# Kernel optimization log

Hardware: AMD Instinct MI355X
Metric: run time of the kernel (lower is better)

Reference implementation:

```python
import jax, jax.numpy as jnp
import numpy as np

E = 1024   # embedding_dim
A = 1024   # attention_dim
H = 16     # num_heads
D = A // H # head_dim


def setup_inputs() -> dict:
    key = jax.random.key(0)
    ks = jax.random.split(key, 9)
    s = 1.0 / np.sqrt(E)
    so = 1.0 / np.sqrt(A)
    return {
        "x": jax.random.normal(ks[0], (2, 2048, E), dtype=jnp.float32),
        "Wq": jax.random.uniform(ks[1], (E, A), jnp.float32, -s, s),
        "bq": jax.random.uniform(ks[2], (A,), jnp.float32, -s, s),
        "Wk": jax.random.uniform(ks[3], (E, A), jnp.float32, -s, s),
        "bk": jax.random.uniform(ks[4], (A,), jnp.float32, -s, s),
        "Wv": jax.random.uniform(ks[5], (E, A), jnp.float32, -s, s),
        "bv": jax.random.uniform(ks[6], (A,), jnp.float32, -s, s),
        "Wo": jax.random.uniform(ks[7], (A, E), jnp.float32, -so, so),
        "bo": jax.random.uniform(ks[8], (E,), jnp.float32, -so, so),
    }


def reference(x, Wq, bq, Wk, bk, Wv, bv, Wo, bo):
    B, S, _ = x.shape
    # projections -> [B, H, S, D]
    def split_heads(t):
        return t.reshape(B, S, H, D).transpose(0, 2, 1, 3)
    Q = split_heads(x @ Wq + bq)
    K = split_heads(x @ Wk + bk)
    V = split_heads(x @ Wv + bv)
    scores = jnp.einsum("bhqd,bhkd->bhqk", Q, K) / jnp.sqrt(jnp.float32(D))
    causal = jnp.tril(jnp.ones((S, S), dtype=bool))
    scores = jnp.where(causal, scores, -jnp.inf)
    attn = jax.nn.softmax(scores, axis=-1)  # dropout p=0 (eval/deterministic)
    ctx = jnp.einsum("bhqk,bhkd->bhqd", attn, V)
    ctx = ctx.transpose(0, 2, 1, 3).reshape(B, S, A)
    out = ctx @ Wo + bo
    return (out, attn)
```

## Files before the change

### kernel.cpp

```cpp
#include <hip/hip_runtime.h>
#include <cstddef>

typedef __bf16 bf16_t;
typedef __attribute__((ext_vector_type(8))) __bf16 bf16x8;
typedef __attribute__((ext_vector_type(4))) float f32x4;

#define BATCH 2
#define SEQ   2048
#define EMB   1024
#define ADIM  1024
#define NHEAD 16
#define HDIM  64
#define MROWS 4096

__device__ inline unsigned short f2bf(float f) {
    bf16_t b = (bf16_t)f;
    return __builtin_bit_cast(unsigned short, b);
}

__global__ __launch_bounds__(256) void convert_x_kernel(
    const float* __restrict__ in, unsigned short* __restrict__ out, int n8)
{
    int i = blockIdx.x * 256 + threadIdx.x;
    if (i >= n8) return;
    const float4* p = (const float4*)(in + (size_t)i * 8);
    float4 a = p[0], b = p[1];
    unsigned int w0 = f2bf(a.x) | ((unsigned)f2bf(a.y) << 16);
    unsigned int w1 = f2bf(a.z) | ((unsigned)f2bf(a.w) << 16);
    unsigned int w2 = f2bf(b.x) | ((unsigned)f2bf(b.y) << 16);
    unsigned int w3 = f2bf(b.z) | ((unsigned)f2bf(b.w) << 16);
    uint4 v = {w0, w1, w2, w3};
    *(uint4*)(out + (size_t)i * 8) = v;
}

__global__ __launch_bounds__(256) void transpose_w_kernel(
    const float* __restrict__ Wq, const float* __restrict__ Wk,
    const float* __restrict__ Wv, const float* __restrict__ Wo,
    unsigned short* __restrict__ Wt_qkv, unsigned short* __restrict__ Wt_o)
{
    __shared__ float tile[64][65];
    const int m = blockIdx.z;
    const float* W = (m == 0) ? Wq : (m == 1) ? Wk : (m == 2) ? Wv : Wo;
    unsigned short* dst = (m < 3) ? (Wt_qkv + (size_t)m * 1024 * 1024) : Wt_o;
    const int r0 = blockIdx.y * 64, c0 = blockIdx.x * 64;
    const int t = threadIdx.x;
    const int r = t >> 2, c4 = (t & 3) * 16;
    #pragma unroll
    for (int j = 0; j < 16; j += 4) {
        float4 v = *(const float4*)(W + (size_t)(r0 + r) * 1024 + c0 + c4 + j);
        tile[r][c4 + j + 0] = v.x;
        tile[r][c4 + j + 1] = v.y;
        tile[r][c4 + j + 2] = v.z;
        tile[r][c4 + j + 3] = v.w;
    }
    __syncthreads();
    const int oc = t >> 2, ch = (t & 3) * 16;
    unsigned int ww[8];
    #pragma unroll
    for (int j = 0; j < 16; j += 2)
        ww[j >> 1] = f2bf(tile[ch + j][oc]) | ((unsigned)f2bf(tile[ch + j + 1][oc]) << 16);
    unsigned short* o = dst + (size_t)(c0 + oc) * 1024 + r0 + ch;
    *(uint4*)(o) = *(uint4*)&ww[0];
    *(uint4*)(o + 8) = *(uint4*)&ww[4];
}

template<int EPI, int NBX, int NWG>
__global__ __launch_bounds__(256) void gemm_mfma_kernel(
    const unsigned short* __restrict__ A,
    const unsigned short* __restrict__ Bt,
    const float* __restrict__ b0, const float* __restrict__ b1, const float* __restrict__ b2,
    void* __restrict__ outp, unsigned short* __restrict__ vt)
{
    __shared__ __align__(16) unsigned short Asm[4096];
    __shared__ __align__(16) unsigned short Bsm[4096];
    const int tid = threadIdx.x, lane = tid & 63, w = tid >> 6;
    const int wr = w >> 1, wc = w & 1;

    const int lin = blockIdx.x;
    const int wg = (lin & 7) * (NWG >> 3) + (lin >> 3);
    const int stripe = wg / (8 * NBX);
    const int rem = wg % (8 * NBX);
    const int bx = rem >> 3;
    const int by = stripe * 8 + (rem & 7);

    const int rowBase = by * 128, colBase = bx * 128;
    const int K = 1024;

    f32x4 acc[4][4];
    #pragma unroll
    for (int i = 0; i < 4; ++i)
        #pragma unroll
        for (int j = 0; j < 4; ++j)
            acc[i][j] = (f32x4){0.f, 0.f, 0.f, 0.f};

    int mt_s[2], cc_s[2], r16_s[2];
    #pragma unroll
    for (int i = 0; i < 2; ++i) {
        int chunk = w * 128 + i * 64 + lane;
        mt_s[i] = chunk >> 6;
        cc_s[i] = (chunk & 63) >> 4;
        r16_s[i] = chunk & 15;
    }

    for (int k0 = 0; k0 < K; k0 += 32) {
        __syncthreads();
        #pragma unroll
        for (int i = 0; i < 2; ++i) {
            const unsigned short* ga = A + (size_t)(rowBase + mt_s[i] * 16 + r16_s[i]) * K + k0 + cc_s[i] * 8;
            __builtin_amdgcn_global_load_lds(
                (const __attribute__((address_space(1))) unsigned int*)ga,
                (__attribute__((address_space(3))) unsigned int*)(Asm + (size_t)(w * 128 + i * 64) * 8),
                16, 0, 0);
            const unsigned short* gb = Bt + (size_t)(colBase + mt_s[i] * 16 + r16_s[i]) * K + k0 + cc_s[i] * 8;
            __builtin_amdgcn_global_load_lds(
                (const __attribute__((address_space(1))) unsigned int*)gb,
                (__attribute__((address_space(3))) unsigned int*)(Bsm + (size_t)(w * 128 + i * 64) * 8),
                16, 0, 0);
        }
        __syncthreads();

        bf16x8 af[4], bfr[4];
        #pragma unroll
        for (int mt = 0; mt < 4; ++mt)
            af[mt] = *(const bf16x8*)(Asm + (size_t)((wr * 4 + mt) * 64 + lane) * 8);
        #pragma unroll
        for (int nt = 0; nt < 4; ++nt)
            bfr[nt] = *(const bf16x8*)(Bsm + (size_t)((wc * 4 + nt) * 64 + lane) * 8);
        #pragma unroll
        for (int mt = 0; mt < 4; ++mt)
            #pragma unroll
            for (int nt = 0; nt < 4; ++nt)
                acc[mt][nt] = __builtin_amdgcn_mfma_f32_16x16x32_bf16(af[mt], bfr[nt], acc[mt][nt], 0, 0, 0);
    }

    const int g = lane >> 4, r16 = lane & 15;
    const int seg = colBase >> 10;
    const float* bias = (seg == 0) ? b0 : (seg == 1) ? b1 : b2;

    if (EPI == 0) {
        unsigned short* qkv = (unsigned short*)outp;
        #pragma unroll
        for (int mt = 0; mt < 4; ++mt) {
            const int row0 = rowBase + wr * 64 + mt * 16 + 4 * g;
            #pragma unroll
            for (int nt = 0; nt < 4; ++nt) {
                const int col = colBase + wc * 64 + nt * 16 + r16;
                const float bb = bias[col & 1023];
                if (seg < 2) {
                    #pragma unroll
                    for (int rr = 0; rr < 4; ++rr)
                        qkv[(size_t)(row0 + rr) * 3072 + col] = f2bf(acc[mt][nt][rr] + bb);
                } else {
                    unsigned int p0 = f2bf(acc[mt][nt][0] + bb) | ((unsigned)f2bf(acc[mt][nt][1] + bb) << 16);
                    unsigned int p1 = f2bf(acc[mt][nt][2] + bb) | ((unsigned)f2bf(acc[mt][nt][3] + bb) << 16);
                    uint2 pv = {p0, p1};
                    *(uint2*)(vt + (size_t)(col - 2048) * 4096 + row0) = pv;
                }
            }
        }
    } else {
        float* out = (float*)outp;
        #pragma unroll
        for (int mt = 0; mt < 4; ++mt) {
            const int row0 = rowBase + wr * 64 + mt * 16 + 4 * g;
            #pragma unroll
            for (int nt = 0; nt < 4; ++nt) {
                const int col = colBase + wc * 64 + nt * 16 + r16;
                const float bb = bias[col];
                #pragma unroll
                for (int rr = 0; rr < 4; ++rr)
                    out[(size_t)(row0 + rr) * 1024 + col] = acc[mt][nt][rr] + bb;
            }
        }
    }
}

__global__ __launch_bounds__(256, 4) void attn_mfma_kernel(
    const unsigned short* __restrict__ qkv,
    const unsigned short* __restrict__ vt,
    float* __restrict__ attn,
    unsigned short* __restrict__ ctx)
{
    __shared__ __align__(16) unsigned short Ksm[2][4096];
    __shared__ __align__(16) unsigned short Vsm[2][4096];
    __shared__ __align__(16) unsigned short Psm[4][1024];

    const int j = blockIdx.x;
    const int xcd = j & 7, slot = j >> 3;
    const int bh = xcd + 8 * (slot & 3);
    const int s4 = slot >> 2;
    const int qt = 8 * (s4 >> 3) + (((s4 & 7) + 2 * (s4 >> 3)) & 7);
    const int b = bh >> 4, h = bh & 15;
    const int tid = threadIdx.x, lane = tid & 63, w = tid >> 6;
    const int g = lane >> 4, r16 = lane & 15;
    const int qrow0 = qt * 64 + w * 16;

    bf16x8 qf[2];
    #pragma unroll
    for (int k2 = 0; k2 < 2; ++k2)
        qf[k2] = *(const bf16x8*)(qkv + (size_t)(b * SEQ + qrow0 + r16) * 3072 + h * 64 + k2 * 32 + g * 8);

    const int sr = tid >> 2;
    const int sbc = (tid & 3) * 32;
    const int swz = (sr & 7) << 4;
    char* Kb = (char*)Ksm;
    char* Vb = (char*)Vsm;

    float rsum[4] = {0.f, 0.f, 0.f, 0.f};

    {
        const char* gk = (const char*)(qkv + (size_t)(b * SEQ + sr) * 3072 + 1024 + h * 64);
        uint4 a0 = *(const uint4*)(gk + sbc);
        uint4 a1 = *(const uint4*)(gk + sbc + 16);
        *(uint4*)(Kb + ((sr * 128 + sbc) ^ swz)) = a0;
        *(uint4*)(Kb + ((sr * 128 + sbc + 16) ^ swz)) = a1;
    }
    __syncthreads();
    for (int kt = 0; kt <= qt; ++kt) {
        const int cur = kt & 1;
        uint4 a0, a1;
        if (kt < qt) {
            const char* gk = (const char*)(qkv + (size_t)(b * SEQ + (kt + 1) * 64 + sr) * 3072 + 1024 + h * 64);
            a0 = *(const uint4*)(gk + sbc);
            a1 = *(const uint4*)(gk + sbc + 16);
        }
        const char* Kc = Kb + cur * 8192;
        #pragma unroll
        for (int nt = 0; nt < 4; ++nt) {
            f32x4 s = {0.f, 0.f, 0.f, 0.f};
            const int krow = nt * 16 + r16;
            #pragma unroll
            for (int k2 = 0; k2 < 2; ++k2) {
                bf16x8 kf = *(const bf16x8*)(Kc + ((krow * 128 + k2 * 64 + g * 16) ^ ((krow & 7) << 4)));
                s = __builtin_amdgcn_mfma_f32_16x16x32_bf16(qf[k2], kf, s, 0, 0, 0);
            }
            #pragma unroll
            for (int rr = 0; rr < 4; ++rr) {
                const int q = qrow0 + 4 * g + rr;
                const int k = kt * 64 + nt * 16 + r16;
                if (k <= q) rsum[rr] += __expf(s[rr] * 0.125f);
            }
        }
        if (kt < qt) {
            char* Kn = Kb + (cur ^ 1) * 8192;
            *(uint4*)(Kn + ((sr * 128 + sbc) ^ swz)) = a0;
            *(uint4*)(Kn + ((sr * 128 + sbc + 16) ^ swz)) = a1;
        }
        __syncthreads();
    }
    #pragma unroll
    for (int rr = 0; rr < 4; ++rr) {
        float v = rsum[rr];
        v += __shfl_xor(v, 1, 64);
        v += __shfl_xor(v, 2, 64);
        v += __shfl_xor(v, 4, 64);
        v += __shfl_xor(v, 8, 64);
        rsum[rr] = 1.0f / v;
    }

    f32x4 cacc[4];
    #pragma unroll
    for (int nt = 0; nt < 4; ++nt) cacc[nt] = (f32x4){0.f, 0.f, 0.f, 0.f};

    {
        const char* gk = (const char*)(qkv + (size_t)(b * SEQ + sr) * 3072 + 1024 + h * 64);
        uint4 a0 = *(const uint4*)(gk + sbc);
        uint4 a1 = *(const uint4*)(gk + sbc + 16);
        const char* gv = (const char*)(vt + (size_t)(h * 64 + sr) * 4096 + b * SEQ);
        uint4 v0 = *(const uint4*)(gv + sbc);
        uint4 v1 = *(const uint4*)(gv + sbc + 16);
        *(uint4*)(Kb + ((sr * 128 + sbc) ^ swz)) = a0;
        *(uint4*)(Kb + ((sr * 128 + sbc + 16) ^ swz)) = a1;
        *(uint4*)(Vb + ((sr * 128 + sbc) ^ swz)) = v0;
        *(uint4*)(Vb + ((sr * 128 + sbc + 16) ^ swz)) = v1;
    }
    __syncthreads();
    for (int kt = 0; kt <= qt; ++kt) {
        const int cur = kt & 1;
        const int kbase = kt * 64;
        uint4 a0, a1, v0, v1;
        if (kt < qt) {
            const char* gk = (const char*)(qkv + (size_t)(b * SEQ + kbase + 64 + sr) * 3072 + 1024 + h * 64);
            a0 = *(const uint4*)(gk + sbc);
            a1 = *(const uint4*)(gk + sbc + 16);
            const char* gv = (const char*)(vt + (size_t)(h * 64 + sr) * 4096 + b * SEQ + kbase + 64);
            v0 = *(const uint4*)(gv + sbc);
            v1 = *(const uint4*)(gv + sbc + 16);
        }
        const char* Kc = Kb + cur * 8192;
        const char* Vc = Vb + cur * 8192;

        #pragma unroll
        for (int nt = 0; nt < 4; ++nt) {
            f32x4 s = {0.f, 0.f, 0.f, 0.f};
            const int krow = nt * 16 + r16;
            #pragma unroll
            for (int k2 = 0; k2 < 2; ++k2) {
                bf16x8 kf = *(const bf16x8*)(Kc + ((krow * 128 + k2 * 64 + g * 16) ^ ((krow & 7) << 4)));
                s = __builtin_amdgcn_mfma_f32_16x16x32_bf16(qf[k2], kf, s, 0, 0, 0);
            }
            #pragma unroll
            for (int rr = 0; rr < 4; ++rr) {
                const int q = qrow0 + 4 * g + rr;
                const int k = kbase + nt * 16 + r16;
                float pn = 0.0f;
                if (k <= q) pn = __expf(s[rr] * 0.125f) * rsum[rr];
                attn[((size_t)bh * SEQ + q) * SEQ + k] = pn;
                const int prow = 4 * g + rr;
                *(unsigned short*)((char*)(Psm[w]) + ((prow * 128 + (nt * 16 + r16) * 2) ^ ((prow & 7) << 4))) = f2bf(pn);
            }
        }
        bf16x8 pf[2];
        #pragma unroll
        for (int k2 = 0; k2 < 2; ++k2)
            pf[k2] = *(const bf16x8*)((char*)(Psm[w]) + ((r16 * 128 + k2 * 64 + g * 16) ^ ((r16 & 7) << 4)));
        #pragma unroll
        for (int nt = 0; nt < 4; ++nt) {
            const int vrow = nt * 16 + r16;
            #pragma unroll
            for (int k2 = 0; k2 < 2; ++k2) {
                bf16x8 vf = *(const bf16x8*)(Vc + ((vrow * 128 + k2 * 64 + g * 16) ^ ((vrow & 7) << 4)));
                cacc[nt] = __builtin_amdgcn_mfma_f32_16x16x32_bf16(pf[k2], vf, cacc[nt], 0, 0, 0);
            }
        }
        if (kt < qt) {
            char* Kn = Kb + (cur ^ 1) * 8192;
            char* Vn = Vb + (cur ^ 1) * 8192;
            *(uint4*)(Kn + ((sr * 128 + sbc) ^ swz)) = a0;
            *(uint4*)(Kn + ((sr * 128 + sbc + 16) ^ swz)) = a1;
            *(uint4*)(Vn + ((sr * 128 + sbc) ^ swz)) = v0;
            *(uint4*)(Vn + ((sr * 128 + sbc + 16) ^ swz)) = v1;
        }
        __syncthreads();
    }

    #pragma unroll
    for (int nt = 0; nt < 4; ++nt)
        #pragma unroll
        for (int rr = 0; rr < 4; ++rr) {
            const int q = qrow0 + 4 * g + rr;
            ctx[(size_t)(b * SEQ + q) * 1024 + h * 64 + nt * 16 + r16] = f2bf(cacc[nt][rr]);
        }

    const int colStart = 64 * (qt + 1);
    const int Wc = SEQ - colStart;
    if (Wc > 0) {
        const int w4 = Wc >> 2;
        for (int c = tid; c < 64 * w4; c += 256) {
            const int row = qt * 64 + c / w4;
            const int col = colStart + (c % w4) * 4;
            *(float4*)(attn + ((size_t)bh * SEQ + row) * SEQ + col) = make_float4(0.f, 0.f, 0.f, 0.f);
        }
    }
}

extern "C" void kernel_launch(void* const* d_in, const int* in_sizes, int n_in,
                              void* d_out, int out_size, void* d_ws, size_t ws_size,
                              hipStream_t stream)
{
    const float* x  = (const float*)d_in[0];
    const float* Wq = (const float*)d_in[1];
    const float* bq = (const float*)d_in[2];
    const float* Wk = (const float*)d_in[3];
    const float* bk = (const float*)d_in[4];
    const float* Wv = (const float*)d_in[5];
    const float* bv = (const float*)d_in[6];
    const float* Wo = (const float*)d_in[7];
    const float* bo = (const float*)d_in[8];

    float* out  = (float*)d_out;
    float* attn = out + (size_t)BATCH * SEQ * EMB;

    unsigned short* xb     = (unsigned short*)d_ws;
    unsigned short* wt_qkv = xb + (size_t)MROWS * 1024;
    unsigned short* wt_o   = wt_qkv + (size_t)3072 * 1024;
    unsigned short* qkvb   = wt_o + (size_t)1024 * 1024;
    unsigned short* vtb    = qkvb + (size_t)MROWS * 3072;
    unsigned short* ctxb   = vtb + (size_t)1024 * MROWS;

    convert_x_kernel<<<2048, 256, 0, stream>>>(x, xb, MROWS * 1024 / 8);
    transpose_w_kernel<<<dim3(16, 16, 4), 256, 0, stream>>>(Wq, Wk, Wv, Wo, wt_qkv, wt_o);

    gemm_mfma_kernel<0, 24, 768><<<768, 256, 0, stream>>>(xb, wt_qkv, bq, bk, bv, qkvb, vtb);

    attn_mfma_kernel<<<1024, 256, 0, stream>>>(qkvb, vtb, attn, ctxb);

    gemm_mfma_kernel<1, 8, 256><<<256, 256, 0, stream>>>(ctxb, wt_o, bo, bo, bo, out, nullptr);
}
```

Baseline: 251.7 us.

## Split softmax row-sum pass into separate key-split kernel

Moves the first pass of the two-pass softmax (QK^T then exp row sums) out of the attention kernel into a new rowsum kernel. That kernel splits the key range into four chunks per query tile across a 3D grid and writes partial sums to workspace. The attention kernel then reads and combines the partials. This parallelises the causal first pass, which was serial and load-imbalanced in each block. In exchange it adds a kernel launch and reads K directly from global memory without LDS staging, and it skips the max-subtraction just as before.

```diff
diff --git a/kernel.cpp b/kernel.cpp
--- a/kernel.cpp
+++ b/kernel.cpp
@@ -175,9 +175,74 @@
     }
 }
 
+__global__ __launch_bounds__(256) void rowsum_kernel(
+    const unsigned short* __restrict__ qkv,
+    float* __restrict__ partial)
+{
+    const int bh = blockIdx.x, qt = blockIdx.y, ks = blockIdx.z;
+    const int b = bh >> 4, h = bh & 15;
+    const int tid = threadIdx.x, lane = tid & 63, w = tid >> 6;
+    const int g = lane >> 4, r16 = lane & 15;
+    float* pbase = partial + (((size_t)(bh * 32 + qt)) * 4 + ks) * 64;
+
+    if (ks * 8 > qt) {
+        if (tid < 64) pbase[tid] = 0.0f;
+        return;
+    }
+
+    const int qrow0 = qt * 64 + w * 16;
+    bf16x8 qf[2];
+    #pragma unroll
+    for (int k2 = 0; k2 < 2; ++k2)
+        qf[k2] = *(const bf16x8*)(qkv + (size_t)(b * SEQ + qrow0 + r16) * 3072 + h * 64 + k2 * 32 + g * 8);
+
+    float rsum[4] = {0.f, 0.f, 0.f, 0.f};
+    const int ktEnd = (ks * 8 + 8 < qt + 1) ? ks * 8 + 8 : qt + 1;
+    for (int kt = ks * 8; kt < ktEnd; ++kt) {
+        const unsigned short* kp = qkv + (size_t)(b * SEQ + kt * 64) * 3072 + 1024 + h * 64;
+        #pragma unroll
+        for (int nt = 0; nt < 4; ++nt) {
+            f32x4 s = {0.f, 0.f, 0.f, 0.f};
+            const int krow = nt * 16 + r16;
+            #pragma unroll
+            for (int k2 = 0; k2 < 2; ++k2) {
+                bf16x8 kf = *(const bf16x8*)(kp + (size_t)krow * 3072 + k2 * 32 + g * 8);
+                s = __builtin_amdgcn_mfma_f32_16x16x32_bf16(qf[k2], kf, s, 0, 0, 0);
+            }
+            if (kt < qt) {
+                #pragma unroll
+                for (int rr = 0; rr < 4; ++rr)
+                    rsum[rr] += __expf(s[rr] * 0.125f);
+            } else {
+                #pragma unroll
+                for (int rr = 0; rr < 4; ++rr) {
+                    const int q = qrow0 + 4 * g + rr;
+                    const int k = kt * 64 + nt * 16 + r16;
+                    if (k <= q) rsum[rr] += __expf(s[rr] * 0.125f);
+                }
+            }
+        }
+    }
+    #pragma unroll
+    for (int rr = 0; rr < 4; ++rr) {
+        float v = rsum[rr];
+        v += __shfl_xor(v, 1, 64);
+        v += __shfl_xor(v, 2, 64);
+        v += __shfl_xor(v, 4, 64);
+        v += __shfl_xor(v, 8, 64);
+        rsum[rr] = v;
+    }
+    if (r16 == 0) {
+        #pragma unroll
+        for (int rr = 0; rr < 4; ++rr)
+            pbase[w * 16 + 4 * g + rr] = rsum[rr];
+    }
+}
+
 __global__ __launch_bounds__(256, 4) void attn_mfma_kernel(
     const unsigned short* __restrict__ qkv,
     const unsigned short* __restrict__ vt,
+    const float* __restrict__ partial,
     float* __restrict__ attn,
     unsigned short* __restrict__ ctx)
 {
@@ -200,63 +265,19 @@
     for (int k2 = 0; k2 < 2; ++k2)
         qf[k2] = *(const bf16x8*)(qkv + (size_t)(b * SEQ + qrow0 + r16) * 3072 + h * 64 + k2 * 32 + g * 8);
 
+    float rsum[4];
+    {
+        const float* pp = partial + ((size_t)(bh * 32 + qt)) * 4 * 64 + w * 16 + 4 * g;
+        #pragma unroll
+        for (int rr = 0; rr < 4; ++rr)
+            rsum[rr] = 1.0f / (pp[rr] + pp[64 + rr] + pp[128 + rr] + pp[192 + rr]);
+    }
+
     const int sr = tid >> 2;
     const int sbc = (tid & 3) * 32;
     const int swz = (sr & 7) << 4;
     char* Kb = (char*)Ksm;
     char* Vb = (char*)Vsm;
-
-    float rsum[4] = {0.f, 0.f, 0.f, 0.f};
-
-    {
-        const char* gk = (const char*)(qkv + (size_t)(b * SEQ + sr) * 3072 + 1024 + h * 64);
-        uint4 a0 = *(const uint4*)(gk + sbc);
-        uint4 a1 = *(const uint4*)(gk + sbc + 16);
-        *(uint4*)(Kb + ((sr * 128 + sbc) ^ swz)) = a0;
-        *(uint4*)(Kb + ((sr * 128 + sbc + 16) ^ swz)) = a1;
-    }
-    __syncthreads();
-    for (int kt = 0; kt <= qt; ++kt) {
-        const int cur = kt & 1;
-        uint4 a0, a1;
-        if (kt < qt) {
-            const char* gk = (const char*)(qkv + (size_t)(b * SEQ + (kt + 1) * 64 + sr) * 3072 + 1024 + h * 64);
-            a0 = *(const uint4*)(gk + sbc);
-            a1 = *(const uint4*)(gk + sbc + 16);
-        }
-        const char* Kc = Kb + cur * 8192;
-        #pragma unroll
-        for (int nt = 0; nt < 4; ++nt) {
-            f32x4 s = {0.f, 0.f, 0.f, 0.f};
-            const int krow = nt * 16 + r16;
-            #pragma unroll
-            for (int k2 = 0; k2 < 2; ++k2) {
-                bf16x8 kf = *(const bf16x8*)(Kc + ((krow * 128 + k2 * 64 + g * 16) ^ ((krow & 7) << 4)));
-                s = __builtin_amdgcn_mfma_f32_16x16x32_bf16(qf[k2], kf, s, 0, 0, 0);
-            }
-            #pragma unroll
-            for (int rr = 0; rr < 4; ++rr) {
-                const int q = qrow0 + 4 * g + rr;
-                const int k = kt * 64 + nt * 16 + r16;
-                if (k <= q) rsum[rr] += __expf(s[rr] * 0.125f);
-            }
-        }
-        if (kt < qt) {
-            char* Kn = Kb + (cur ^ 1) * 8192;
-            *(uint4*)(Kn + ((sr * 128 + sbc) ^ swz)) = a0;
-            *(uint4*)(Kn + ((sr * 128 + sbc + 16) ^ swz)) = a1;
-        }
-        __syncthreads();
-    }
-    #pragma unroll
-    for (int rr = 0; rr < 4; ++rr) {
-        float v = rsum[rr];
-        v += __shfl_xor(v, 1, 64);
-        v += __shfl_xor(v, 2, 64);
-        v += __shfl_xor(v, 4, 64);
-        v += __shfl_xor(v, 8, 64);
-        rsum[rr] = 1.0f / v;
-    }
 
     f32x4 cacc[4];
     #pragma unroll
@@ -377,13 +398,16 @@
     unsigned short* qkvb   = wt_o + (size_t)1024 * 1024;
     unsigned short* vtb    = qkvb + (size_t)MROWS * 3072;
     unsigned short* ctxb   = vtb + (size_t)1024 * MROWS;
+    float* rsp             = (float*)(ctxb + (size_t)MROWS * 1024);
 
     convert_x_kernel<<<2048, 256, 0, stream>>>(x, xb, MROWS * 1024 / 8);
     transpose_w_kernel<<<dim3(16, 16, 4), 256, 0, stream>>>(Wq, Wk, Wv, Wo, wt_qkv, wt_o);
 
     gemm_mfma_kernel<0, 24, 768><<<768, 256, 0, stream>>>(xb, wt_qkv, bq, bk, bv, qkvb, vtb);
 
-    attn_mfma_kernel<<<1024, 256, 0, stream>>>(qkvb, vtb, attn, ctxb);
+    rowsum_kernel<<<dim3(32, 32, 4), 256, 0, stream>>>(qkvb, rsp);
+
+    attn_mfma_kernel<<<1024, 256, 0, stream>>>(qkvb, vtb, rsp, attn, ctxb);
 
     gemm_mfma_kernel<1, 8, 256><<<256, 256, 0, stream>>>(ctxb, wt_o, bo, bo, bo, out, nullptr);
 }
```

Result: slower. 346.1 us (+37.5%).

## Widen attention blocks to 128 query rows sharing each K/V tile

Applied to the files above, without the earlier changes.

The attention kernel now uses 512 threads (8 waves) per block, covering 128 query rows instead of 64, so each staged K/V tile in shared memory serves twice as many query rows. Each thread loads one 16-byte chunk per tile instead of two. Block-to-tile mapping is changed to pair ascending and descending query tiles across the two grid halves to balance the causal workload. The trade-offs are fewer blocks (512), lower occupancy per CU, and extra diagonal-tile work for the larger query tile.

```diff
diff --git a/kernel.cpp b/kernel.cpp
--- a/kernel.cpp
+++ b/kernel.cpp
@@ -175,7 +175,7 @@
     }
 }
 
-__global__ __launch_bounds__(256, 4) void attn_mfma_kernel(
+__global__ __launch_bounds__(512, 2) void attn_mfma_kernel(
     const unsigned short* __restrict__ qkv,
     const unsigned short* __restrict__ vt,
     float* __restrict__ attn,
@@ -183,25 +183,28 @@
 {
     __shared__ __align__(16) unsigned short Ksm[2][4096];
     __shared__ __align__(16) unsigned short Vsm[2][4096];
-    __shared__ __align__(16) unsigned short Psm[4][1024];
+    __shared__ __align__(16) unsigned short Psm[8][1024];
 
     const int j = blockIdx.x;
-    const int xcd = j & 7, slot = j >> 3;
-    const int bh = xcd + 8 * (slot & 3);
-    const int s4 = slot >> 2;
-    const int qt = 8 * (s4 >> 3) + (((s4 & 7) + 2 * (s4 >> 3)) & 7);
+    const int half = j >> 8;
+    const int r = j & 255;
+    const int xcd = r & 7, s = r >> 3;
+    const int bh = xcd + 8 * (s & 3);
+    const int qtl = s >> 2;
+    const int qt = half ? (15 - qtl) : qtl;
     const int b = bh >> 4, h = bh & 15;
     const int tid = threadIdx.x, lane = tid & 63, w = tid >> 6;
     const int g = lane >> 4, r16 = lane & 15;
-    const int qrow0 = qt * 64 + w * 16;
+    const int qrow0 = qt * 128 + w * 16;
+    const int ktMax = 2 * qt + 1;
 
     bf16x8 qf[2];
     #pragma unroll
     for (int k2 = 0; k2 < 2; ++k2)
         qf[k2] = *(const bf16x8*)(qkv + (size_t)(b * SEQ + qrow0 + r16) * 3072 + h * 64 + k2 * 32 + g * 8);
 
-    const int sr = tid >> 2;
-    const int sbc = (tid & 3) * 32;
+    const int sr = tid >> 3;
+    const int sbc = (tid & 7) * 16;
     const int swz = (sr & 7) << 4;
     char* Kb = (char*)Ksm;
     char* Vb = (char*)Vsm;
@@ -211,40 +214,36 @@
     {
         const char* gk = (const char*)(qkv + (size_t)(b * SEQ + sr) * 3072 + 1024 + h * 64);
         uint4 a0 = *(const uint4*)(gk + sbc);
-        uint4 a1 = *(const uint4*)(gk + sbc + 16);
         *(uint4*)(Kb + ((sr * 128 + sbc) ^ swz)) = a0;
-        *(uint4*)(Kb + ((sr * 128 + sbc + 16) ^ swz)) = a1;
     }
     __syncthreads();
-    for (int kt = 0; kt <= qt; ++kt) {
+    for (int kt = 0; kt <= ktMax; ++kt) {
         const int cur = kt & 1;
-        uint4 a0, a1;
-        if (kt < qt) {
+        uint4 a0;
+        if (kt < ktMax) {
             const char* gk = (const char*)(qkv + (size_t)(b * SEQ + (kt + 1) * 64 + sr) * 3072 + 1024 + h * 64);
             a0 = *(const uint4*)(gk + sbc);
-            a1 = *(const uint4*)(gk + sbc + 16);
         }
         const char* Kc = Kb + cur * 8192;
         #pragma unroll
         for (int nt = 0; nt < 4; ++nt) {
-            f32x4 s = {0.f, 0.f, 0.f, 0.f};
+            f32x4 sc = {0.f, 0.f, 0.f, 0.f};
             const int krow = nt * 16 + r16;
             #pragma unroll
             for (int k2 = 0; k2 < 2; ++k2) {
                 bf16x8 kf = *(const bf16x8*)(Kc + ((krow * 128 + k2 * 64 + g * 16) ^ ((krow & 7) << 4)));
-                s = __builtin_amdgcn_mfma_f32_16x16x32_bf16(qf[k2], kf, s, 0, 0, 0);
+                sc = __builtin_amdgcn_mfma_f32_16x16x32_bf16(qf[k2], kf, sc, 0, 0, 0);
             }
             #pragma unroll
             for (int rr = 0; rr < 4; ++rr) {
                 const int q = qrow0 + 4 * g + rr;
                 const int k = kt * 64 + nt * 16 + r16;
-                if (k <= q) rsum[rr] += __expf(s[rr] * 0.125f);
-            }
-        }
-        if (kt < qt) {
+                if (k <= q) rsum[rr] += __expf(sc[rr] * 0.125f);
+            }
+        }
+        if (kt < ktMax) {
             char* Kn = Kb + (cur ^ 1) * 8192;
             *(uint4*)(Kn + ((sr * 128 + sbc) ^ swz)) = a0;
-            *(uint4*)(Kn + ((sr * 128 + sbc + 16) ^ swz)) = a1;
         }
         __syncthreads();
     }
@@ -265,46 +264,41 @@
     {
         const char* gk = (const char*)(qkv + (size_t)(b * SEQ + sr) * 3072 + 1024 + h * 64);
         uint4 a0 = *(const uint4*)(gk + sbc);
-        uint4 a1 = *(const uint4*)(gk + sbc + 16);
         const char* gv = (const char*)(vt + (size_t)(h * 64 + sr) * 4096 + b * SEQ);
         uint4 v0 = *(const uint4*)(gv + sbc);
-        uint4 v1 = *(const uint4*)(gv + sbc + 16);
+        __syncthreads();
         *(uint4*)(Kb + ((sr * 128 + sbc) ^ swz)) = a0;
-        *(uint4*)(Kb + ((sr * 128 + sbc + 16) ^ swz)) = a1;
         *(uint4*)(Vb + ((sr * 128 + sbc) ^ swz)) = v0;
-        *(uint4*)(Vb + ((sr * 128 + sbc + 16) ^ swz)) = v1;
     }
     __syncthreads();
-    for (int kt = 0; kt <= qt; ++kt) {
+    for (int kt = 0; kt <= ktMax; ++kt) {
         const int cur = kt & 1;
         const int kbase = kt * 64;
-        uint4 a0, a1, v0, v1;
-        if (kt < qt) {
+        uint4 a0, v0;
+        if (kt < ktMax) {
             const char* gk = (const char*)(qkv + (size_t)(b * SEQ + kbase + 64 + sr) * 3072 + 1024 + h * 64);
             a0 = *(const uint4*)(gk + sbc);
-            a1 = *(const uint4*)(gk + sbc + 16);
             const char* gv = (const char*)(vt + (size_t)(h * 64 + sr) * 4096 + b * SEQ + kbase + 64);
             v0 = *(const uint4*)(gv + sbc);
-            v1 = *(const uint4*)(gv + sbc + 16);
         }
         const char* Kc = Kb + cur * 8192;
         const char* Vc = Vb + cur * 8192;
 
         #pragma unroll
         for (int nt = 0; nt < 4; ++nt) {
-            f32x4 s = {0.f, 0.f, 0.f, 0.f};
+            f32x4 sc = {0.f, 0.f, 0.f, 0.f};
             const int krow = nt * 16 + r16;
             #pragma unroll
             for (int k2 = 0; k2 < 2; ++k2) {
                 bf16x8 kf = *(const bf16x8*)(Kc + ((krow * 128 + k2 * 64 + g * 16) ^ ((krow & 7) << 4)));
-                s = __builtin_amdgcn_mfma_f32_16x16x32_bf16(qf[k2], kf, s, 0, 0, 0);
+                sc = __builtin_amdgcn_mfma_f32_16x16x32_bf16(qf[k2], kf, sc, 0, 0, 0);
             }
             #pragma unroll
             for (int rr = 0; rr < 4; ++rr) {
                 const int q = qrow0 + 4 * g + rr;
                 const int k = kbase + nt * 16 + r16;
                 float pn = 0.0f;
-                if (k <= q) pn = __expf(s[rr] * 0.125f) * rsum[rr];
+                if (k <= q) pn = __expf(sc[rr] * 0.125f) * rsum[rr];
                 attn[((size_t)bh * SEQ + q) * SEQ + k] = pn;
                 const int prow = 4 * g + rr;
                 *(unsigned short*)((char*)(Psm[w]) + ((prow * 128 + (nt * 16 + r16) * 2) ^ ((prow & 7) << 4))) = f2bf(pn);
@@ -323,13 +317,11 @@
                 cacc[nt] = __builtin_amdgcn_mfma_f32_16x16x32_bf16(pf[k2], vf, cacc[nt], 0, 0, 0);
             }
         }
-        if (kt < qt) {
+        if (kt < ktMax) {
             char* Kn = Kb + (cur ^ 1) * 8192;
             char* Vn = Vb + (cur ^ 1) * 8192;
             *(uint4*)(Kn + ((sr * 128 + sbc) ^ swz)) = a0;
-            *(uint4*)(Kn + ((sr * 128 + sbc + 16) ^ swz)) = a1;
             *(uint4*)(Vn + ((sr * 128 + sbc) ^ swz)) = v0;
-            *(uint4*)(Vn + ((sr * 128 + sbc + 16) ^ swz)) = v1;
         }
         __syncthreads();
     }
@@ -342,12 +334,12 @@
             ctx[(size_t)(b * SEQ + q) * 1024 + h * 64 + nt * 16 + r16] = f2bf(cacc[nt][rr]);
         }
 
-    const int colStart = 64 * (qt + 1);
+    const int colStart = 128 * (qt + 1);
     const int Wc = SEQ - colStart;
     if (Wc > 0) {
         const int w4 = Wc >> 2;
-        for (int c = tid; c < 64 * w4; c += 256) {
-            const int row = qt * 64 + c / w4;
+        for (int c = tid; c < 128 * w4; c += 512) {
+            const int row = qt * 128 + c / w4;
             const int col = colStart + (c % w4) * 4;
             *(float4*)(attn + ((size_t)bh * SEQ + row) * SEQ + col) = make_float4(0.f, 0.f, 0.f, 0.f);
         }
@@ -383,7 +375,7 @@
 
     gemm_mfma_kernel<0, 24, 768><<<768, 256, 0, stream>>>(xb, wt_qkv, bq, bk, bv, qkvb, vtb);
 
-    attn_mfma_kernel<<<1024, 256, 0, stream>>>(qkvb, vtb, attn, ctxb);
+    attn_mfma_kernel<<<512, 512, 0, stream>>>(qkvb, vtb, attn, ctxb);
 
     gemm_mfma_kernel<1, 8, 256><<<256, 256, 0, stream>>>(ctxb, wt_o, bo, bo, bo, out, nullptr);
 }
```

Measured after the change: 300.3 us. 19.3% more time.

## Process two K tiles per barrier in row-sum pass using V buffer as extra stages

Applied to the files above, without the earlier changes.

The softmax-denominator pass now keeps four K tiles in shared memory by borrowing the V buffers as two extra stages. Each iteration computes two key tiles and prefetches the next two, which halves the number of __syncthreads and deepens the global-load prefetch. In exchange it uses more registers for the prefetched data and adds conditional buffer-selection logic, and it depends on the V shared buffers being unused during this pass.

```diff
diff --git a/kernel.cpp b/kernel.cpp
--- a/kernel.cpp
+++ b/kernel.cpp
@@ -209,42 +209,65 @@
     float rsum[4] = {0.f, 0.f, 0.f, 0.f};
 
     {
-        const char* gk = (const char*)(qkv + (size_t)(b * SEQ + sr) * 3072 + 1024 + h * 64);
-        uint4 a0 = *(const uint4*)(gk + sbc);
-        uint4 a1 = *(const uint4*)(gk + sbc + 16);
-        *(uint4*)(Kb + ((sr * 128 + sbc) ^ swz)) = a0;
-        *(uint4*)(Kb + ((sr * 128 + sbc + 16) ^ swz)) = a1;
+        const char* gk0 = (const char*)(qkv + (size_t)(b * SEQ + sr) * 3072 + 1024 + h * 64);
+        uint4 p0 = *(const uint4*)(gk0 + sbc);
+        uint4 p1 = *(const uint4*)(gk0 + sbc + 16);
+        *(uint4*)(Kb + ((sr * 128 + sbc) ^ swz)) = p0;
+        *(uint4*)(Kb + ((sr * 128 + sbc + 16) ^ swz)) = p1;
+        if (qt >= 1) {
+            const char* gk1 = (const char*)(qkv + (size_t)(b * SEQ + 64 + sr) * 3072 + 1024 + h * 64);
+            uint4 q0 = *(const uint4*)(gk1 + sbc);
+            uint4 q1 = *(const uint4*)(gk1 + sbc + 16);
+            *(uint4*)(Kb + 8192 + ((sr * 128 + sbc) ^ swz)) = q0;
+            *(uint4*)(Kb + 8192 + ((sr * 128 + sbc + 16) ^ swz)) = q1;
+        }
     }
     __syncthreads();
-    for (int kt = 0; kt <= qt; ++kt) {
-        const int cur = kt & 1;
-        uint4 a0, a1;
-        if (kt < qt) {
-            const char* gk = (const char*)(qkv + (size_t)(b * SEQ + (kt + 1) * 64 + sr) * 3072 + 1024 + h * 64);
+    for (int t0 = 0; t0 <= qt; t0 += 2) {
+        uint4 a0, a1, c0, c1;
+        const bool pf2 = (t0 + 2 <= qt), pf3 = (t0 + 3 <= qt);
+        if (pf2) {
+            const char* gk = (const char*)(qkv + (size_t)(b * SEQ + (t0 + 2) * 64 + sr) * 3072 + 1024 + h * 64);
             a0 = *(const uint4*)(gk + sbc);
             a1 = *(const uint4*)(gk + sbc + 16);
         }
-        const char* Kc = Kb + cur * 8192;
-        #pragma unroll
-        for (int nt = 0; nt < 4; ++nt) {
-            f32x4 s = {0.f, 0.f, 0.f, 0.f};
-            const int krow = nt * 16 + r16;
-            #pragma unroll
-            for (int k2 = 0; k2 < 2; ++k2) {
-                bf16x8 kf = *(const bf16x8*)(Kc + ((krow * 128 + k2 * 64 + g * 16) ^ ((krow & 7) << 4)));
-                s = __builtin_amdgcn_mfma_f32_16x16x32_bf16(qf[k2], kf, s, 0, 0, 0);
-            }
-            #pragma unroll
-            for (int rr = 0; rr < 4; ++rr) {
-                const int q = qrow0 + 4 * g + rr;
-                const int k = kt * 64 + nt * 16 + r16;
-                if (k <= q) rsum[rr] += __expf(s[rr] * 0.125f);
-            }
-        }
-        if (kt < qt) {
-            char* Kn = Kb + (cur ^ 1) * 8192;
-            *(uint4*)(Kn + ((sr * 128 + sbc) ^ swz)) = a0;
-            *(uint4*)(Kn + ((sr * 128 + sbc + 16) ^ swz)) = a1;
+        if (pf3) {
+            const char* gk = (const char*)(qkv + (size_t)(b * SEQ + (t0 + 3) * 64 + sr) * 3072 + 1024 + h * 64);
+            c0 = *(const uint4*)(gk + sbc);
+            c1 = *(const uint4*)(gk + sbc + 16);
+        }
+        #pragma unroll
+        for (int sub = 0; sub < 2; ++sub) {
+            const int kt = t0 + sub;
+            if (kt <= qt) {
+                const char* Kc = ((kt & 2) ? Vb : Kb) + (kt & 1) * 8192;
+                #pragma unroll
+                for (int nt = 0; nt < 4; ++nt) {
+                    f32x4 s = {0.f, 0.f, 0.f, 0.f};
+                    const int krow = nt * 16 + r16;
+                    #pragma unroll
+                    for (int k2 = 0; k2 < 2; ++k2) {
+                        bf16x8 kf = *(const bf16x8*)(Kc + ((krow * 128 + k2 * 64 + g * 16) ^ ((krow & 7) << 4)));
+                        s = __builtin_amdgcn_mfma_f32_16x16x32_bf16(qf[k2], kf, s, 0, 0, 0);
+                    }
+                    #pragma unroll
+                    for (int rr = 0; rr < 4; ++rr) {
+                        const int q = qrow0 + 4 * g + rr;
+                        const int k = kt * 64 + nt * 16 + r16;
+                        if (k <= q) rsum[rr] += __expf(s[rr] * 0.125f);
+                    }
+                }
+            }
+        }
+        if (pf2) {
+            char* dstp = (((t0 + 2) & 2) ? Vb : Kb) + ((t0 + 2) & 1) * 8192;
+            *(uint4*)(dstp + ((sr * 128 + sbc) ^ swz)) = a0;
+            *(uint4*)(dstp + ((sr * 128 + sbc + 16) ^ swz)) = a1;
+        }
+        if (pf3) {
+            char* dstp = (((t0 + 3) & 2) ? Vb : Kb) + ((t0 + 3) & 1) * 8192;
+            *(uint4*)(dstp + ((sr * 128 + sbc) ^ swz)) = c0;
+            *(uint4*)(dstp + ((sr * 128 + sbc + 16) ^ swz)) = c1;
         }
         __syncthreads();
     }
```

After: 248.6 us. No clear change (-1.2%).
